# Performance work log

Hardware: AMD Instinct MI355X
Metric: run time of the kernel (lower is better)

Reference implementation:

```python
import jax, jax.numpy as jnp
import numpy as np

N_FEAT = 32
EPS = 1e-7


def _normalize_gate(g1, g2, g3):
    s = jnp.abs(g1) + jnp.abs(g2) + jnp.abs(g3) + EPS
    m = (s >= 1.0).astype(g1.dtype)
    norm = lambda g: (1.0 - m) * g + m * (g / s)
    return norm(g1), norm(g2), norm(g3)


def _gate_recurrent(xm, g1, g2, g3, horizontal, reverse):
    """SPN GateRecurrent2dnoind. xm,g*: [B,C,H,W].
    h(t) = (1-g1-g2-g3)*x(t) + g1*h_prev(k-1) + g2*h_prev(k) + g3*h_prev(k+1),
    scanned over W (horizontal) or H (vertical); out-of-range h := 0.
    """
    if horizontal:
        perm, inv = (3, 0, 1, 2), (1, 2, 3, 0)   # [W,B,C,H], cross dim = H
    else:
        perm, inv = (2, 0, 1, 3), (1, 2, 0, 3)   # [H,B,C,W], cross dim = W
    xt = jnp.transpose(xm, perm)
    a = jnp.transpose(g1, perm)
    b = jnp.transpose(g2, perm)
    c = jnp.transpose(g3, perm)

    def step(h, inp):
        x_t, a_t, b_t, c_t = inp
        zero = jnp.zeros_like(h[..., :1])
        h_m = jnp.concatenate([zero, h[..., :-1]], axis=-1)  # h_prev(k-1)
        h_p = jnp.concatenate([h[..., 1:], zero], axis=-1)   # h_prev(k+1)
        h_new = (1.0 - a_t - b_t - c_t) * x_t + a_t * h_m + b_t * h + c_t * h_p
        return h_new, h_new

    init = jnp.zeros_like(xt[0])
    _, ys = jax.lax.scan(step, init, (xt, a, b, c), reverse=reverse)
    return jnp.transpose(ys, inv)


def setup_inputs() -> dict:
    key = jax.random.key(0)
    k1, k2 = jax.random.split(key)
    x = jax.random.normal(k1, (4, 12 * N_FEAT, 256, 256), dtype=jnp.float32)
    mask = jax.random.normal(k2, (4, N_FEAT, 256, 256), dtype=jnp.float32)
    return {"x": x, "mask": mask}


def reference(x, mask):
    nf = N_FEAT
    gs = [x[:, k * nf:(k + 1) * nf] for k in range(12)]
    outs = []
    dirs = [(True, False), (True, True), (False, False), (False, True)]
    for d, (horiz, rev) in enumerate(dirs):
        g1, g2, g3 = _normalize_gate(gs[3 * d], gs[3 * d + 1], gs[3 * d + 2])
        outs.append(_gate_recurrent(mask, g1, g2, g3, horiz, rev))
    return jnp.maximum(jnp.maximum(outs[0], outs[1]), jnp.maximum(outs[2], outs[3]))
```

## Files before the change

kernel.cpp:

```cpp
#include <hip/hip_runtime.h>

#define HW 256
#define NF 32
#define TCOLS 8

__device__ __forceinline__ unsigned enc(float f) {
  unsigned u = __float_as_uint(f);
  return u ^ (0x80000000u | (unsigned)((int)u >> 31));
}
__device__ __forceinline__ float dec(unsigned k) {
  unsigned b = (k & 0x80000000u) ? (k ^ 0x80000000u) : ~k;
  return __uint_as_float(b);
}

__device__ __forceinline__ float4 mk4(float a, float b, float c, float d) {
  float4 v; v.x = a; v.y = b; v.z = c; v.w = d; return v;
}

__device__ __forceinline__ float stepf(float a, float b, float c, float xm,
                                       float hm, float hc, float hp) {
  float s = fabsf(a) + fabsf(b) + fabsf(c) + 1e-7f;
  float inv = __builtin_amdgcn_rcpf(s);
  if (s < 1.0f) inv = 1.0f;
  a *= inv; b *= inv; c *= inv;
  float h = (1.0f - a - b - c) * xm;
  h = fmaf(a, hm, h);
  h = fmaf(b, hc, h);
  h = fmaf(c, hp, h);
  return h;
}


#define COL_STEP(jj)                                                        \
  {                                                                         \
    const float4 A  = *(const float4*)&tl[0][jj][4 * lane];                 \
    const float4 Bv = *(const float4*)&tl[1][jj][4 * lane];                 \
    const float4 Cv = *(const float4*)&tl[2][jj][4 * lane];                 \
    const float4 X  = *(const float4*)&tl[3][jj][4 * lane];                 \
    float left = __shfl_up(hv.w, 1);                                        \
    if (lane == 0) left = 0.f;                                              \
    float right = __shfl_down(hv.x, 1);                                     \
    if (lane == 63) right = 0.f;                                            \
    float4 hn;                                                              \
    hn.x = stepf(A.x, Bv.x, Cv.x, X.x, left, hv.x, hv.y);                   \
    hn.y = stepf(A.y, Bv.y, Cv.y, X.y, hv.x, hv.y, hv.z);                   \
    hn.z = stepf(A.z, Bv.z, Cv.z, X.z, hv.y, hv.z, hv.w);                   \
    hn.w = stepf(A.w, Bv.w, Cv.w, X.w, hv.z, hv.w, right);                  \
    res[jj] = hn;                                                           \
    hv = hn;                                                                \
  }

__global__ __launch_bounds__(64, 1) void spn_scan_ws(
    const float* __restrict__ x, const float* __restrict__ mask,
    float* __restrict__ ws) {
  const int bid = blockIdx.x;
  const int lane = threadIdx.x;
  const size_t plane = (size_t)HW * HW;
  const size_t PBUF = (size_t)4 * NF * plane;

  if (bid < 256) {
    __shared__ float tl[4][TCOLS][HW];
    const int dir = bid >> 7;
    const int rem = bid & 127;
    const int b = rem >> 5, ch = rem & 31;
    const bool rev = (dir == 1);
    const float* g1p = x + ((size_t)b * 12 * NF + (3 * dir + 0) * NF + ch) * plane;
    const float* g2p = x + ((size_t)b * 12 * NF + (3 * dir + 1) * NF + ch) * plane;
    const float* g3p = x + ((size_t)b * 12 * NF + (3 * dir + 2) * NF + ch) * plane;
    const float* mp  = mask + ((size_t)b * NF + ch) * plane;
    float* wdir = ws + (size_t)dir * PBUF + ((size_t)b * NF + ch) * plane;
    const float* ps[4] = {g1p, g2p, g3p, mp};

    const int r_lo = lane >> 1;
    const int c0 = (lane & 1) * 4;
    float4 Pr[32];
    float4 hv = mk4(0.f, 0.f, 0.f, 0.f);

    int t0 = rev ? (HW - TCOLS) : 0;
#pragma unroll
    for (int q = 0; q < 32; ++q) {
      const int p = q >> 3, pass = q & 7;
      Pr[q] = *(const float4*)(ps[p] + (size_t)(pass * 32 + r_lo) * HW + t0 + c0);
    }

    for (int k = 0; k < HW / TCOLS; ++k) {
#pragma unroll
      for (int q = 0; q < 32; ++q) {
        const int p = q >> 3, pass = q & 7;
        const int r = pass * 32 + r_lo;
        tl[p][c0 + 0][r] = Pr[q].x;
        tl[p][c0 + 1][r] = Pr[q].y;
        tl[p][c0 + 2][r] = Pr[q].z;
        tl[p][c0 + 3][r] = Pr[q].w;
      }
      const int t0c = t0;
      t0 += rev ? -TCOLS : TCOLS;
      if (k + 1 < HW / TCOLS) {
#pragma unroll
        for (int q = 0; q < 32; ++q) {
          const int p = q >> 3, pass = q & 7;
          Pr[q] = *(const float4*)(ps[p] + (size_t)(pass * 32 + r_lo) * HW + t0 + c0);
        }
      }
      asm volatile("s_waitcnt lgkmcnt(0)" ::: "memory");

      float4 res[TCOLS];
      if (!rev) {
        COL_STEP(0) COL_STEP(1) COL_STEP(2) COL_STEP(3)
        COL_STEP(4) COL_STEP(5) COL_STEP(6) COL_STEP(7)
      } else {
        COL_STEP(7) COL_STEP(6) COL_STEP(5) COL_STEP(4)
        COL_STEP(3) COL_STEP(2) COL_STEP(1) COL_STEP(0)
      }

      float* wr = wdir + (size_t)(4 * lane) * HW + t0c;
      *(float4*)(wr)              = mk4(res[0].x, res[1].x, res[2].x, res[3].x);
      *(float4*)(wr + 4)          = mk4(res[4].x, res[5].x, res[6].x, res[7].x);
      *(float4*)(wr + HW)         = mk4(res[0].y, res[1].y, res[2].y, res[3].y);
      *(float4*)(wr + HW + 4)     = mk4(res[4].y, res[5].y, res[6].y, res[7].y);
      *(float4*)(wr + 2 * HW)     = mk4(res[0].z, res[1].z, res[2].z, res[3].z);
      *(float4*)(wr + 2 * HW + 4) = mk4(res[4].z, res[5].z, res[6].z, res[7].z);
      *(float4*)(wr + 3 * HW)     = mk4(res[0].w, res[1].w, res[2].w, res[3].w);
      *(float4*)(wr + 3 * HW + 4) = mk4(res[4].w, res[5].w, res[6].w, res[7].w);
    }
  } else {
    const int sid = bid - 256;
    const int dir = 2 + (sid >> 7);
    const int rem = sid & 127;
    const int b = rem >> 5, ch = rem & 31;
    const bool rev = (dir == 3);
    const float* g1p = x + ((size_t)b * 12 * NF + (3 * dir + 0) * NF + ch) * plane;
    const float* g2p = x + ((size_t)b * 12 * NF + (3 * dir + 1) * NF + ch) * plane;
    const float* g3p = x + ((size_t)b * 12 * NF + (3 * dir + 2) * NF + ch) * plane;
    const float* mp  = mask + ((size_t)b * NF + ch) * plane;
    float* wdir = ws + (size_t)dir * PBUF + ((size_t)b * NF + ch) * plane;

    const int koff = lane * 4;
    float4 hv = mk4(0.f, 0.f, 0.f, 0.f);
    float4 Ab[4], Bb[4], Cb[4], Xb[4];
#pragma unroll
    for (int p = 0; p < 4; ++p) {
      const int t = rev ? (HW - 1 - p) : p;
      const size_t ro = (size_t)t * HW + koff;
      Ab[p] = *(const float4*)(g1p + ro);
      Bb[p] = *(const float4*)(g2p + ro);
      Cb[p] = *(const float4*)(g3p + ro);
      Xb[p] = *(const float4*)(mp + ro);
    }

#define VSTEP(s, ph)                                                        \
  {                                                                         \
    const int t = rev ? (HW - 1 - (s)) : (s);                               \
    const float4 A = Ab[ph], Bv = Bb[ph], Cv = Cb[ph], X = Xb[ph];          \
    float left = __shfl_up(hv.w, 1);                                        \
    if (lane == 0) left = 0.f;                                              \
    float right = __shfl_down(hv.x, 1);                                     \
    if (lane == 63) right = 0.f;                                            \
    float4 hn;                                                              \
    hn.x = stepf(A.x, Bv.x, Cv.x, X.x, left, hv.x, hv.y);                   \
    hn.y = stepf(A.y, Bv.y, Cv.y, X.y, hv.x, hv.y, hv.z);                   \
    hn.z = stepf(A.z, Bv.z, Cv.z, X.z, hv.y, hv.z, hv.w);                   \
    hn.w = stepf(A.w, Bv.w, Cv.w, X.w, hv.z, hv.w, right);                  \
    *(float4*)(wdir + (size_t)t * HW + koff) = hn;                          \
    const int sn = (s) + 4;                                                 \
    if (sn < HW) {                                                          \
      const int tn = rev ? (HW - 1 - sn) : sn;                              \
      const size_t ro = (size_t)tn * HW + koff;                             \
      Ab[ph] = *(const float4*)(g1p + ro);                                  \
      Bb[ph] = *(const float4*)(g2p + ro);                                  \
      Cb[ph] = *(const float4*)(g3p + ro);                                  \
      Xb[ph] = *(const float4*)(mp + ro);                                   \
    }                                                                       \
    hv = hn;                                                                \
  }

    for (int s = 0; s < HW; s += 4) {
      VSTEP(s + 0, 0);
      VSTEP(s + 1, 1);
      VSTEP(s + 2, 2);
      VSTEP(s + 3, 3);
    }
#undef VSTEP
  }
}

__global__ __launch_bounds__(256) void spn_combine(
    const float4* __restrict__ w0, const float4* __restrict__ w1,
    const float4* __restrict__ w2, const float4* __restrict__ w3,
    float4* __restrict__ o) {
  const int i = blockIdx.x * 256 + threadIdx.x;
  const float4 a = w0[i], b = w1[i], c = w2[i], d = w3[i];
  float4 r;
  r.x = fmaxf(fmaxf(a.x, b.x), fmaxf(c.x, d.x));
  r.y = fmaxf(fmaxf(a.y, b.y), fmaxf(c.y, d.y));
  r.z = fmaxf(fmaxf(a.z, b.z), fmaxf(c.z, d.z));
  r.w = fmaxf(fmaxf(a.w, b.w), fmaxf(c.w, d.w));
  o[i] = r;
}

__global__ __launch_bounds__(256) void spn_scan_atomic(
    const float* __restrict__ x, const float* __restrict__ mask,
    unsigned* __restrict__ out) {
  const int bid = blockIdx.x;
  const int tid = threadIdx.x;
  __shared__ float tl[4][TCOLS][HW];
  __shared__ float hb[2][HW + 2];
  const size_t plane = (size_t)HW * HW;

  if (bid < 256) {
    const int dir = bid >> 7;
    const int rem = bid & 127;
    const int b = rem >> 5, ch = rem & 31;
    const bool rev = (dir == 1);
    const float* g1p = x + ((size_t)b * 12 * NF + (3 * dir + 0) * NF + ch) * plane;
    const float* g2p = x + ((size_t)b * 12 * NF + (3 * dir + 1) * NF + ch) * plane;
    const float* g3p = x + ((size_t)b * 12 * NF + (3 * dir + 2) * NF + ch) * plane;
    const float* mp  = mask + ((size_t)b * NF + ch) * plane;
    unsigned* op = out + ((size_t)b * NF + ch) * plane;

    for (int i = tid; i < 2 * (HW + 2); i += 256) (&hb[0][0])[i] = 0.0f;

    float hreg = 0.0f;
    int cur = 0;
    const int r0 = tid >> 1, cc = tid & 1;
    const float* ps[4] = {g1p, g2p, g3p, mp};
    for (int tile = 0; tile < HW / TCOLS; ++tile) {
      const int t0 = rev ? (HW - TCOLS - tile * TCOLS) : (tile * TCOLS);
      __syncthreads();
#pragma unroll
      for (int p = 0; p < 4; ++p) {
#pragma unroll
        for (int half = 0; half < 2; ++half) {
          const int r = r0 + half * 128;
          const float4 v = *(const float4*)(ps[p] + (size_t)r * HW + t0 + cc * 4);
          tl[p][cc * 4 + 0][r] = v.x;
          tl[p][cc * 4 + 1][r] = v.y;
          tl[p][cc * 4 + 2][r] = v.z;
          tl[p][cc * 4 + 3][r] = v.w;
        }
      }
      __syncthreads();
      for (int j = 0; j < TCOLS; ++j) {
        const int col = rev ? (TCOLS - 1 - j) : j;
        const int t = t0 + col;
        const float a  = tl[0][col][tid];
        const float g2 = tl[1][col][tid];
        const float c  = tl[2][col][tid];
        const float xm = tl[3][col][tid];
        const float hm = hb[cur][tid];
        const float hp = hb[cur][tid + 2];
        const float h = stepf(a, g2, c, xm, hm, hreg, hp);
        hb[cur ^ 1][tid + 1] = h;
        hreg = h;
        atomicMax(op + (size_t)tid * HW + t, enc(h));
        __syncthreads();
        cur ^= 1;
      }
    }
  } else {
    if (tid >= 64) return;
    const int lane = tid;
    const int vb = bid - 256;
    const int dir = 2 + (vb >> 7);
    const int rem = vb & 127;
    const int b = rem >> 5, ch = rem & 31;
    const bool rev = (dir == 3);
    const float* g1p = x + ((size_t)b * 12 * NF + (3 * dir + 0) * NF + ch) * plane;
    const float* g2p = x + ((size_t)b * 12 * NF + (3 * dir + 1) * NF + ch) * plane;
    const float* g3p = x + ((size_t)b * 12 * NF + (3 * dir + 2) * NF + ch) * plane;
    const float* mp  = mask + ((size_t)b * NF + ch) * plane;
    unsigned* op = out + ((size_t)b * NF + ch) * plane;

    float4 hv = {0.f, 0.f, 0.f, 0.f};
    int t = rev ? (HW - 1) : 0;
    const int koff = lane * 4;
    float4 a4 = *(const float4*)(g1p + (size_t)t * HW + koff);
    float4 b4 = *(const float4*)(g2p + (size_t)t * HW + koff);
    float4 c4 = *(const float4*)(g3p + (size_t)t * HW + koff);
    float4 x4 = *(const float4*)(mp  + (size_t)t * HW + koff);
    for (int step = 0; step < HW; ++step) {
      const float4 A = a4, B = b4, C = c4, X = x4;
      const int tn = rev ? (HW - 2 - step) : (step + 1);
      if (step + 1 < HW) {
        a4 = *(const float4*)(g1p + (size_t)tn * HW + koff);
        b4 = *(const float4*)(g2p + (size_t)tn * HW + koff);
        c4 = *(const float4*)(g3p + (size_t)tn * HW + koff);
        x4 = *(const float4*)(mp  + (size_t)tn * HW + koff);
      }
      float left = __shfl_up(hv.w, 1);
      if (lane == 0) left = 0.f;
      float right = __shfl_down(hv.x, 1);
      if (lane == 63) right = 0.f;
      float4 hn;
      hn.x = stepf(A.x, B.x, C.x, X.x, left, hv.x, hv.y);
      hn.y = stepf(A.y, B.y, C.y, X.y, hv.x, hv.y, hv.z);
      hn.z = stepf(A.z, B.z, C.z, X.z, hv.y, hv.z, hv.w);
      hn.w = stepf(A.w, B.w, C.w, X.w, hv.z, hv.w, right);
      unsigned* o = op + (size_t)t * HW + koff;
      atomicMax(o + 0, enc(hn.x));
      atomicMax(o + 1, enc(hn.y));
      atomicMax(o + 2, enc(hn.z));
      atomicMax(o + 3, enc(hn.w));
      hv = hn;
      t = tn;
    }
  }
}

__global__ __launch_bounds__(256) void spn_decode(unsigned* __restrict__ o) {
  const int i = blockIdx.x * 256 + threadIdx.x;
  uint4 v = ((uint4*)o)[i];
  float4 f;
  f.x = dec(v.x); f.y = dec(v.y); f.z = dec(v.z); f.w = dec(v.w);
  ((float4*)o)[i] = f;
}

extern "C" void kernel_launch(void* const* d_in, const int* in_sizes, int n_in,
                              void* d_out, int out_size, void* d_ws, size_t ws_size,
                              hipStream_t stream) {
  const float* x = (const float*)d_in[0];
  const float* mask = (const float*)d_in[1];
  (void)in_sizes; (void)n_in;
  const size_t need = (size_t)4 * out_size * sizeof(float);
  if (ws_size >= need) {
    float* ws = (float*)d_ws;
    spn_scan_ws<<<512, 64, 0, stream>>>(x, mask, ws);
    spn_combine<<<out_size / 1024, 256, 0, stream>>>(
        (const float4*)ws, (const float4*)(ws + (size_t)out_size),
        (const float4*)(ws + 2 * (size_t)out_size),
        (const float4*)(ws + 3 * (size_t)out_size), (float4*)d_out);
  } else {
    hipMemsetAsync(d_out, 0, (size_t)out_size * sizeof(float), stream);
    spn_scan_atomic<<<512, 256, 0, stream>>>(x, mask, (unsigned*)d_out);
    spn_decode<<<out_size / 1024, 256, 0, stream>>>((unsigned*)d_out);
  }
}
```

Measured before the change: 750.5 us.

## Stage horizontal-scan tiles via async global_load_lds double buffering with swizzle

The horizontal-direction scan now stages each 8-column tile straight from global memory into a double-buffered LDS array using global_load_lds. Loads for the next tile are issued before computing the current one, and vmcnt waits gate their use. This replaces the register-staged Pr[32] prefetch and the transposing LDS scatter stores. An XOR swizzle on the staging lanes and read offsets is meant to avoid bank conflicts when each lane reads its 4 rows as float4. The change frees many registers and removes the LDS write pass, but it relies on correct vmcnt accounting and there is no explicit barrier, which is safe only because the block is a single wavefront.

Measured after the change: 747.8 us. About the same (-0.4%).

```diff
diff --git a/kernel.cpp b/kernel.cpp
--- a/kernel.cpp
+++ b/kernel.cpp
@@ -1,8 +1,10 @@
 #include <hip/hip_runtime.h>
+#include <stdint.h>
 
 #define HW 256
 #define NF 32
 #define TCOLS 8
+#define NT (HW / TCOLS)
 
 __device__ __forceinline__ unsigned enc(float f) {
   unsigned u = __float_as_uint(f);
@@ -30,24 +32,66 @@
   return h;
 }
 
-
-#define COL_STEP(jj)                                                        \
+#define EL_0(v) (v).x
+#define EL_1(v) (v).y
+#define EL_2(v) (v).z
+#define EL_3(v) (v).w
+#define EL(v, cc) EL_##cc(v)
+
+__device__ __forceinline__ void stage_tile(const float* const* ps,
+                                           float (*B)[4][2048], int par,
+                                           int t0, int srow, int scol) {
+#pragma unroll
+  for (int p = 0; p < 4; ++p) {
+#pragma unroll
+    for (int P = 0; P < 8; ++P) {
+      const float* g = ps[p] + (size_t)(P * 32 + srow) * HW + t0 + scol;
+      __builtin_amdgcn_global_load_lds(
+          (const __attribute__((address_space(1))) uint32_t*)g,
+          (__attribute__((address_space(3))) uint32_t*)&B[par][p][P * 256],
+          16, 0, 0);
+    }
+  }
+}
+
+
+#define COLF(jg, cc)                                                        \
   {                                                                         \
-    const float4 A  = *(const float4*)&tl[0][jj][4 * lane];                 \
-    const float4 Bv = *(const float4*)&tl[1][jj][4 * lane];                 \
-    const float4 Cv = *(const float4*)&tl[2][jj][4 * lane];                 \
-    const float4 X  = *(const float4*)&tl[3][jj][4 * lane];                 \
     float left = __shfl_up(hv.w, 1);                                        \
     if (lane == 0) left = 0.f;                                              \
     float right = __shfl_down(hv.x, 1);                                     \
     if (lane == 63) right = 0.f;                                            \
     float4 hn;                                                              \
-    hn.x = stepf(A.x, Bv.x, Cv.x, X.x, left, hv.x, hv.y);                   \
-    hn.y = stepf(A.y, Bv.y, Cv.y, X.y, hv.x, hv.y, hv.z);                   \
-    hn.z = stepf(A.z, Bv.z, Cv.z, X.z, hv.y, hv.z, hv.w);                   \
-    hn.w = stepf(A.w, Bv.w, Cv.w, X.w, hv.z, hv.w, right);                  \
-    res[jj] = hn;                                                           \
+    hn.x = stepf(EL(fa0, cc), EL(fb0, cc), EL(fc0, cc), EL(fx0, cc), left, hv.x, hv.y);  \
+    hn.y = stepf(EL(fa1, cc), EL(fb1, cc), EL(fc1, cc), EL(fx1, cc), hv.x, hv.y, hv.z);  \
+    hn.z = stepf(EL(fa2, cc), EL(fb2, cc), EL(fc2, cc), EL(fx2, cc), hv.y, hv.z, hv.w);  \
+    hn.w = stepf(EL(fa3, cc), EL(fb3, cc), EL(fc3, cc), EL(fx3, cc), hv.z, hv.w, right); \
+    res[(jg) * 4 + (cc)] = hn;                                              \
     hv = hn;                                                                \
+  }
+
+#define LOADG(par, jg)                                                      \
+  {                                                                         \
+    const char* b0 = (const char*)&B[par][0][0];                            \
+    const char* b1 = (const char*)&B[par][1][0];                            \
+    const char* b2 = (const char*)&B[par][2][0];                            \
+    const char* b3 = (const char*)&B[par][3][0];                            \
+    fa0 = *(const float4*)(b0 + rb[0][jg]);                                 \
+    fa1 = *(const float4*)(b0 + rb[1][jg]);                                 \
+    fa2 = *(const float4*)(b0 + rb[2][jg]);                                 \
+    fa3 = *(const float4*)(b0 + rb[3][jg]);                                 \
+    fb0 = *(const float4*)(b1 + rb[0][jg]);                                 \
+    fb1 = *(const float4*)(b1 + rb[1][jg]);                                 \
+    fb2 = *(const float4*)(b1 + rb[2][jg]);                                 \
+    fb3 = *(const float4*)(b1 + rb[3][jg]);                                 \
+    fc0 = *(const float4*)(b2 + rb[0][jg]);                                 \
+    fc1 = *(const float4*)(b2 + rb[1][jg]);                                 \
+    fc2 = *(const float4*)(b2 + rb[2][jg]);                                 \
+    fc3 = *(const float4*)(b2 + rb[3][jg]);                                 \
+    fx0 = *(const float4*)(b3 + rb[0][jg]);                                 \
+    fx1 = *(const float4*)(b3 + rb[1][jg]);                                 \
+    fx2 = *(const float4*)(b3 + rb[2][jg]);                                 \
+    fx3 = *(const float4*)(b3 + rb[3][jg]);                                 \
   }
 
 __global__ __launch_bounds__(64, 1) void spn_scan_ws(
@@ -57,9 +101,9 @@
   const int lane = threadIdx.x;
   const size_t plane = (size_t)HW * HW;
   const size_t PBUF = (size_t)4 * NF * plane;
+  __shared__ __align__(16) float B[2][4][2048];
 
   if (bid < 256) {
-    __shared__ float tl[4][TCOLS][HW];
     const int dir = bid >> 7;
     const int rem = bid & 127;
     const int b = rem >> 5, ch = rem & 31;
@@ -71,48 +115,47 @@
     float* wdir = ws + (size_t)dir * PBUF + ((size_t)b * NF + ch) * plane;
     const float* ps[4] = {g1p, g2p, g3p, mp};
 
-    const int r_lo = lane >> 1;
-    const int c0 = (lane & 1) * 4;
-    float4 Pr[32];
+    const int lp = lane ^ ((lane >> 3) & 7);
+    const int srow = lp >> 1;
+    const int scol = (lp & 1) * 4;
+
+    int rb[4][2];
+#pragma unroll
+    for (int i = 0; i < 4; ++i)
+#pragma unroll
+      for (int jg = 0; jg < 2; ++jg)
+        rb[i][jg] = ((8 * lane + 2 * i + jg) ^ (lane & 7)) * 16;
+
     float4 hv = mk4(0.f, 0.f, 0.f, 0.f);
-
-    int t0 = rev ? (HW - TCOLS) : 0;
-#pragma unroll
-    for (int q = 0; q < 32; ++q) {
-      const int p = q >> 3, pass = q & 7;
-      Pr[q] = *(const float4*)(ps[p] + (size_t)(pass * 32 + r_lo) * HW + t0 + c0);
-    }
-
-    for (int k = 0; k < HW / TCOLS; ++k) {
-#pragma unroll
-      for (int q = 0; q < 32; ++q) {
-        const int p = q >> 3, pass = q & 7;
-        const int r = pass * 32 + r_lo;
-        tl[p][c0 + 0][r] = Pr[q].x;
-        tl[p][c0 + 1][r] = Pr[q].y;
-        tl[p][c0 + 2][r] = Pr[q].z;
-        tl[p][c0 + 3][r] = Pr[q].w;
-      }
-      const int t0c = t0;
-      t0 += rev ? -TCOLS : TCOLS;
-      if (k + 1 < HW / TCOLS) {
-#pragma unroll
-        for (int q = 0; q < 32; ++q) {
-          const int p = q >> 3, pass = q & 7;
-          Pr[q] = *(const float4*)(ps[p] + (size_t)(pass * 32 + r_lo) * HW + t0 + c0);
-        }
-      }
-      asm volatile("s_waitcnt lgkmcnt(0)" ::: "memory");
-
-      float4 res[TCOLS];
+    float4 res[TCOLS];
+    float4 fa0, fa1, fa2, fa3, fb0, fb1, fb2, fb3;
+    float4 fc0, fc1, fc2, fc3, fx0, fx1, fx2, fx3;
+
+    stage_tile(ps, B, 0, rev ? (HW - TCOLS) : 0, srow, scol);
+
+    for (int k = 0; k < NT; ++k) {
+      const int par = k & 1;
+      if (k == 0) {
+        asm volatile("s_waitcnt vmcnt(0)" ::: "memory");
+      } else {
+        asm volatile("s_waitcnt vmcnt(8)" ::: "memory");
+      }
+      __builtin_amdgcn_sched_barrier(0);
+      if (k + 1 < NT) {
+        const int t0n = rev ? (HW - TCOLS - (k + 1) * TCOLS) : ((k + 1) * TCOLS);
+        stage_tile(ps, B, par ^ 1, t0n, srow, scol);
+      }
+      __builtin_amdgcn_sched_barrier(0);
+
       if (!rev) {
-        COL_STEP(0) COL_STEP(1) COL_STEP(2) COL_STEP(3)
-        COL_STEP(4) COL_STEP(5) COL_STEP(6) COL_STEP(7)
+        LOADG(par, 0); COLF(0, 0) COLF(0, 1) COLF(0, 2) COLF(0, 3)
+        LOADG(par, 1); COLF(1, 0) COLF(1, 1) COLF(1, 2) COLF(1, 3)
       } else {
-        COL_STEP(7) COL_STEP(6) COL_STEP(5) COL_STEP(4)
-        COL_STEP(3) COL_STEP(2) COL_STEP(1) COL_STEP(0)
-      }
-
+        LOADG(par, 1); COLF(1, 3) COLF(1, 2) COLF(1, 1) COLF(1, 0)
+        LOADG(par, 0); COLF(0, 3) COLF(0, 2) COLF(0, 1) COLF(0, 0)
+      }
+
+      const int t0c = rev ? (HW - TCOLS - k * TCOLS) : (k * TCOLS);
       float* wr = wdir + (size_t)(4 * lane) * HW + t0c;
       *(float4*)(wr)              = mk4(res[0].x, res[1].x, res[2].x, res[3].x);
       *(float4*)(wr + 4)          = mk4(res[4].x, res[5].x, res[6].x, res[7].x);
```
